# Performance work log

Hardware: AMD Instinct MI355X
Metric: run time of the kernel (lower is better)

Reference implementation:

```python
import jax, jax.numpy as jnp
import numpy as np

NEG_SLOPE = 0.2  # PyG GATConv default negative_slope


def gat_conv(x, src, dst, num_nodes, W, att_src, att_dst, bias, heads, out_ch, concat):
    """PyG-style GATConv (eval mode, self-loops already included in src/dst).
    x: [N, in]; W: [in, heads*out_ch]; att_*: [heads, out_ch]; bias: [heads*out_ch] or [out_ch].
    """
    N = num_nodes
    h = (x @ W).reshape(N, heads, out_ch)                      # [N, H, C]
    a_src = jnp.sum(h * att_src[None], axis=-1)                 # [N, H]
    a_dst = jnp.sum(h * att_dst[None], axis=-1)                 # [N, H]
    e = a_src[src] + a_dst[dst]                                 # [E, H]
    e = jnp.where(e > 0, e, NEG_SLOPE * e)                      # leaky_relu
    # segment softmax over incoming edges of each destination node
    m = jax.ops.segment_max(e, dst, num_segments=N)             # [N, H]
    w = jnp.exp(e - m[dst])                                     # [E, H]
    denom = jax.ops.segment_sum(w, dst, num_segments=N)         # [N, H]
    alpha = w / denom[dst]                                      # [E, H]
    out = jax.ops.segment_sum(h[src] * alpha[:, :, None], dst, num_segments=N)  # [N, H, C]
    if concat:
        out = out.reshape(N, heads * out_ch)
    else:
        out = out.mean(axis=1)
    return out + bias


def setup_inputs() -> dict:
    key = jax.random.key(0)
    ks = jax.random.split(key, 20)
    N, T, F_IN = 100000, 50, 10
    E = 1600000
    H1, C1 = 4, 32          # conv1: heads=4, hidden=32 -> 128
    LAT = 64                # latent_dim

    def g(k, shape, scale):
        return (jax.random.normal(k, shape, dtype=jnp.float32) * scale)

    inp = {
        "temporal_data": jax.random.normal(ks[0], (N, T, F_IN), dtype=jnp.float32),
        "x": jax.random.normal(ks[1], (N, F_IN), dtype=jnp.float32),
        "edge_index": jax.random.randint(ks[2], (2, E), 0, N, dtype=jnp.int32),
        # temporal encoder: Linear(10,64) -> ReLU -> Linear(64,64)
        "tW1": g(ks[3], (F_IN, 64), 0.3), "tb1": jnp.zeros((64,), jnp.float32),
        "tW2": g(ks[4], (64, LAT), 0.12), "tb2": jnp.zeros((LAT,), jnp.float32),
        # GATConv1: in=10, out=32, heads=4, concat
        "gW1": g(ks[5], (F_IN, H1 * C1), 0.3),
        "ga1_src": g(ks[6], (H1, C1), 0.17), "ga1_dst": g(ks[7], (H1, C1), 0.17),
        "gb1": jnp.zeros((H1 * C1,), jnp.float32),
        # GATConv2: in=128, out=64, heads=1, concat=False
        "gW2": g(ks[8], (H1 * C1, LAT), 0.09),
        "ga2_src": g(ks[9], (1, LAT), 0.12), "ga2_dst": g(ks[10], (1, LAT), 0.12),
        "gb2": jnp.zeros((LAT,), jnp.float32),
        # classifier: Linear(128,64) -> ReLU -> (Dropout eval) -> Linear(64,1) -> Sigmoid
        "cW1": g(ks[11], (2 * LAT, 64), 0.09), "cb1": jnp.zeros((64,), jnp.float32),
        "cW2": g(ks[12], (64, 1), 0.12), "cb2": jnp.zeros((1,), jnp.float32),
    }
    return inp


def reference(temporal_data, x, edge_index, tW1, tb1, tW2, tb2,
              gW1, ga1_src, ga1_dst, gb1, gW2, ga2_src, ga2_dst, gb2,
              cW1, cb1, cW2, cb2):
    N = x.shape[0]
    # temporal encoder then mean over time axis (dim=1)
    t = jax.nn.relu(temporal_data @ tW1 + tb1) @ tW2 + tb2      # [N, T, 64]
    t = t.mean(axis=1)                                           # [N, 64]
    # add self-loops (PyG GATConv default add_self_loops=True)
    loop = jnp.arange(N, dtype=edge_index.dtype)
    src = jnp.concatenate([edge_index[0], loop])
    dst = jnp.concatenate([edge_index[1], loop])
    h = gat_conv(x, src, dst, N, gW1, ga1_src, ga1_dst, gb1, heads=4, out_ch=32, concat=True)
    h = jax.nn.elu(h)
    g = gat_conv(h, src, dst, N, gW2, ga2_src, ga2_dst, gb2, heads=1, out_ch=64, concat=False)  # [N, 64]
    combined = jnp.concatenate([t, g], axis=-1)                  # [N, 128]
    z = jax.nn.relu(combined @ cW1 + cb1) @ cW2 + cb2            # [N, 1]
    return jax.nn.sigmoid(z)
```

## Files before the change

### kernel.cpp

```cpp
#include <hip/hip_runtime.h>
#include <hip/hip_bf16.h>

#define DEV_INLINE __device__ __forceinline__

typedef __attribute__((ext_vector_type(8))) short short8v;
typedef __attribute__((ext_vector_type(4))) float f32x4;

DEV_INLINE float lrelu(float v) { return fmaxf(v, 0.2f * v); }

DEV_INLINE unsigned int cvt_pk_bf16(float lo, float hi) {
    unsigned int r;
    asm("v_cvt_pk_bf16_f32 %0, %1, %2" : "=v"(r) : "v"(lo), "v"(hi));
    return r;
}

DEV_INLINE unsigned short f2bf_rne(float f) {
    unsigned int b = __float_as_uint(f);
    return (unsigned short)((b + 0x7FFFu + ((b >> 16) & 1u)) >> 16);
}

DEV_INLINE unsigned int pack_bf16(float lo, float hi) {
    return (unsigned int)f2bf_rne(lo) | ((unsigned int)f2bf_rne(hi) << 16);
}

DEV_INLINE float bf_lo(unsigned int u) { return __uint_as_float(u << 16); }
DEV_INLINE float bf_hi(unsigned int u) { return __uint_as_float(u & 0xFFFF0000u); }

__global__ __launch_bounds__(1024) void k_scan1(const int* __restrict__ counts,
                                                int* __restrict__ rowptr,
                                                int* __restrict__ partials, int N) {
    __shared__ int sd[1024];
    int li = threadIdx.x;
    int i  = blockIdx.x * 1024 + li;
    int v  = (i < N) ? counts[i] : 0;
    sd[li] = v;
    __syncthreads();
    for (int off = 1; off < 1024; off <<= 1) {
        int t = (li >= off) ? sd[li - off] : 0;
        __syncthreads();
        sd[li] += t;
        __syncthreads();
    }
    int inc = sd[li];
    if (i < N) rowptr[i + 1] = inc;
    if (li == 1023) partials[blockIdx.x] = inc;
}

__global__ void k_scan3(int* __restrict__ rowptr, const int* __restrict__ partials,
                        int* __restrict__ nxt, int N) {
    int i = blockIdx.x * blockDim.x + threadIdx.x;
    if (i > N) return;
    int v;
    if (i == 0) { v = 0; rowptr[0] = 0; }
    else {
        int blk = (i - 1) >> 10;
        int pp = 0;
        for (int b = 0; b < blk; ++b) pp += partials[b];
        v = rowptr[i] + pp;
        rowptr[i] = v;
    }
    if (i < N) nxt[i] = v;
}

#define SC_K 8
#define SC_P 16
__global__ __launch_bounds__(256) void k_scatter(const int* __restrict__ ei,
                                                 int* __restrict__ nxt,
                                                 int* __restrict__ col,
                                                 int E, int range) {
    int t = threadIdx.x;
    int base = blockIdx.x * (256 * SC_K);
    int s[SC_K], d[SC_K];
#pragma unroll
    for (int k = 0; k < SC_K; ++k) {
        int e = base + k * 256 + t;
        bool v = (e < E);
        s[k] = v ? ei[e] : 0;
        d[k] = v ? ei[E + e] : -1;
    }
    int lo = 0;
    for (int p = 0; p < SC_P; ++p, lo += range) {
        int hi = lo + range;
#pragma unroll
        for (int k = 0; k < SC_K; ++k) {
            if (d[k] >= lo && d[k] < hi) {
                int pos = atomicAdd(&nxt[d[k]], 1);
                col[pos] = s[k];
            }
        }
        __syncthreads();
    }
}

__global__ __launch_bounds__(256) void k_temporal(const float* __restrict__ td,
                                                  const float* __restrict__ tW1,
                                                  const float* __restrict__ tb1,
                                                  const int* __restrict__ ei,
                                                  int* __restrict__ counts,
                                                  const float* __restrict__ tW2,
                                                  const float* __restrict__ cW1,
                                                  const float* __restrict__ tb2,
                                                  const float* __restrict__ cb1,
                                                  unsigned short* __restrict__ Wf,
                                                  float* __restrict__ bcf,
                                                  unsigned short* __restrict__ mb,
                                                  int N, int E) {
    __shared__ float lds[4][512];
    int tid = threadIdx.x, lane = tid & 63, wv = tid >> 6;
    int gid = blockIdx.x * 256 + tid;

    int estr = gridDim.x * 256;
    for (int e = gid; e < E; e += estr) atomicAdd(&counts[ei[E + e]], 1);

    if (gid < 4096) {
        int i = gid >> 6, c = gid & 63;
        float s = 0.f;
#pragma unroll 8
        for (int k = 0; k < 64; ++k) s = fmaf(tW2[i * 64 + k], cW1[k * 64 + c], s);
        Wf[gid] = f2bf_rne(s);
    } else if (gid < 8192) {
        Wf[gid] = f2bf_rne(cW1[gid]);
    } else if (gid < 8256) {
        int c = gid - 8192;
        float s = cb1[c];
#pragma unroll 8
        for (int k = 0; k < 64; ++k) s = fmaf(tb2[k], cW1[k * 64 + c], s);
        bcf[c] = s;
    }

    int wid  = blockIdx.x * 4 + wv;
    int nwav = gridDim.x * 4;
    int col  = lane & 15;
    int g    = lane >> 4;

    int chunk = (N + nwav - 1) / nwav;
    int n0 = wid * chunk;
    int n1 = min(n0 + chunk, N);
    if (n0 >= n1) return;

    short8v B[4];
#pragma unroll
    for (int cb = 0; cb < 4; ++cb) {
        union { short8v v; unsigned short u[8]; } bu;
#pragma unroll
        for (int j = 0; j < 8; ++j) {
            int f = g * 8 + j;
            int c = cb * 16 + col;
            float w = (f < 10) ? tW1[f * 64 + c] : ((f == 10) ? tb1[c] : 0.f);
            bu.u[j] = f2bf_rne(w);
        }
        B[cb] = bu.v;
    }

    float* wb = lds[wv];

    const float4* r4 = reinterpret_cast<const float4*>(td + (size_t)n0 * 500);
    float4 va = r4[lane];
    float4 vb = (lane < 61) ? r4[64 + lane] : make_float4(0.f, 0.f, 0.f, 0.f);

    for (int n = n0; n < n1; ++n) {
        *reinterpret_cast<float4*>(wb + 4 * lane) = va;
        if (lane < 61) *reinterpret_cast<float4*>(wb + 256 + 4 * lane) = vb;

        if (n + 1 < n1) {
            const float4* rn = reinterpret_cast<const float4*>(td + (size_t)(n + 1) * 500);
            va = rn[lane];
            if (lane < 61) vb = rn[64 + lane];
        }

        float sum0 = 0.f, sum1 = 0.f, sum2 = 0.f, sum3 = 0.f;
#pragma unroll
        for (int tt = 0; tt < 4; ++tt) {
            int t = tt * 16 + col;
            bool valid = (t < 50);
            float x0 = 0.f, x1 = 0.f, x2 = 0.f, x3 = 0.f;
            float x4 = 0.f, x5 = 0.f, x6 = 0.f, x7 = 0.f;
            const float* rp = wb + t * 10;
            if (g == 0 && valid) {
                float2 p0 = *reinterpret_cast<const float2*>(rp);
                float2 p1 = *reinterpret_cast<const float2*>(rp + 2);
                float2 p2 = *reinterpret_cast<const float2*>(rp + 4);
                float2 p3 = *reinterpret_cast<const float2*>(rp + 6);
                x0 = p0.x; x1 = p0.y; x2 = p1.x; x3 = p1.y;
                x4 = p2.x; x5 = p2.y; x6 = p3.x; x7 = p3.y;
            } else if (g == 1 && valid) {
                float2 p4 = *reinterpret_cast<const float2*>(rp + 8);
                x0 = p4.x; x1 = p4.y; x2 = 1.0f;
            }
            union { short8v v; unsigned int w[4]; } au;
            au.w[0] = cvt_pk_bf16(x0, x1);
            au.w[1] = cvt_pk_bf16(x2, x3);
            au.w[2] = cvt_pk_bf16(x4, x5);
            au.w[3] = cvt_pk_bf16(x6, x7);

            f32x4 z = {0.f, 0.f, 0.f, 0.f};
            f32x4 c0 = __builtin_amdgcn_mfma_f32_16x16x32_bf16(au.v, B[0], z, 0, 0, 0);
            f32x4 c1 = __builtin_amdgcn_mfma_f32_16x16x32_bf16(au.v, B[1], z, 0, 0, 0);
            f32x4 c2 = __builtin_amdgcn_mfma_f32_16x16x32_bf16(au.v, B[2], z, 0, 0, 0);
            f32x4 c3 = __builtin_amdgcn_mfma_f32_16x16x32_bf16(au.v, B[3], z, 0, 0, 0);
#pragma unroll
            for (int i = 0; i < 4; ++i) {
                sum0 += fmaxf(c0[i], 0.f);
                sum1 += fmaxf(c1[i], 0.f);
                sum2 += fmaxf(c2[i], 0.f);
                sum3 += fmaxf(c3[i], 0.f);
            }
        }
        sum0 += __shfl_xor(sum0, 16); sum0 += __shfl_xor(sum0, 32);
        sum1 += __shfl_xor(sum1, 16); sum1 += __shfl_xor(sum1, 32);
        sum2 += __shfl_xor(sum2, 16); sum2 += __shfl_xor(sum2, 32);
        sum3 += __shfl_xor(sum3, 16); sum3 += __shfl_xor(sum3, 32);
        float mv = (g == 0) ? sum0 : (g == 1) ? sum1 : (g == 2) ? sum2 : sum3;
        mb[(size_t)n * 64 + lane] = f2bf_rne(mv * 0.02f);
    }
}

__global__ __launch_bounds__(256) void k_g1a(const float* __restrict__ x,
                                             const float* __restrict__ gW1,
                                             const float* __restrict__ as_w,
                                             const float* __restrict__ ad_w,
                                             unsigned short* __restrict__ h1b,
                                             float* __restrict__ a1s,
                                             float* __restrict__ a1d, int N) {
    int tid = threadIdx.x, lane = tid & 63;
    int n0 = blockIdx.x * 4 + (tid >> 6);
    int n  = __builtin_amdgcn_readfirstlane(n0 < N ? n0 : N - 1);

    float wa[10], wb[10];
#pragma unroll
    for (int i = 0; i < 10; ++i) { wa[i] = gW1[i * 128 + lane]; wb[i] = gW1[i * 128 + 64 + lane]; }
    const float* xp = x + (size_t)n * 10;
    float ha = 0.f, hb = 0.f;
#pragma unroll
    for (int i = 0; i < 10; ++i) { float xv = xp[i]; ha = fmaf(xv, wa[i], ha); hb = fmaf(xv, wb[i], hb); }

    int c = lane & 31;
    int headA = lane >> 5;
    float ps_a = ha * as_w[headA * 32 + c];
    float ps_b = hb * as_w[(headA + 2) * 32 + c];
    float pd_a = ha * ad_w[headA * 32 + c];
    float pd_b = hb * ad_w[(headA + 2) * 32 + c];
#pragma unroll
    for (int m = 1; m < 32; m <<= 1) {
        ps_a += __shfl_xor(ps_a, m); ps_b += __shfl_xor(ps_b, m);
        pd_a += __shfl_xor(pd_a, m); pd_b += __shfl_xor(pd_b, m);
    }
    if (n0 < N) {
        h1b[(size_t)n * 128 + lane]      = f2bf_rne(ha);
        h1b[(size_t)n * 128 + 64 + lane] = f2bf_rne(hb);
        if (c == 0) {
            a1s[n * 4 + headA]     = ps_a;
            a1s[n * 4 + 2 + headA] = ps_b;
            a1d[n * 4 + headA]     = pd_a;
            a1d[n * 4 + 2 + headA] = pd_b;
        }
    }
}

__global__ __launch_bounds__(256) void k_g1b(const int* __restrict__ rowptr,
                                             const int* __restrict__ col,
                                             const unsigned int* __restrict__ h1u,
                                             const float* __restrict__ a1s,
                                             const float* __restrict__ a1d,
                                             const float* __restrict__ gb1,
                                             unsigned int* __restrict__ out1u, int N) {
    int tid = threadIdx.x, lane = tid & 63;
    int n0 = blockIdx.x * 4 + (tid >> 6);
    int n  = __builtin_amdgcn_readfirstlane(n0 < N ? n0 : N - 1);

    int start = rowptr[n], end = rowptr[n + 1];
    int h = lane >> 5;
    int c = lane & 31;
    int hsel = c >> 3;
    float advh = a1d[n * 4 + hsel];
    const uint2* h1u2 = reinterpret_cast<const uint2*>(h1u);

    float den = 0.f, a0 = 0.f, a1v = 0.f, a2v = 0.f, a3v = 0.f;
    if (h == 0) {
        float w = __expf(lrelu(a1s[n * 4 + hsel] + advh));
        uint2 u = h1u2[(size_t)n * 32 + c];
        den = w;
        a0 = w * bf_lo(u.x); a1v = w * bf_hi(u.x);
        a2v = w * bf_lo(u.y); a3v = w * bf_hi(u.y);
    }
    int e = start + h;
    for (; e + 2 < end; e += 4) {
        int s0 = col[e], s1 = col[e + 2];
        float q0 = a1s[s0 * 4 + hsel];
        float q1 = a1s[s1 * 4 + hsel];
        uint2 u0 = h1u2[(size_t)s0 * 32 + c];
        uint2 u1 = h1u2[(size_t)s1 * 32 + c];
        float w0 = __expf(lrelu(q0 + advh));
        float w1 = __expf(lrelu(q1 + advh));
        den += w0 + w1;
        a0 = fmaf(w0, bf_lo(u0.x), a0); a1v = fmaf(w0, bf_hi(u0.x), a1v);
        a2v = fmaf(w0, bf_lo(u0.y), a2v); a3v = fmaf(w0, bf_hi(u0.y), a3v);
        a0 = fmaf(w1, bf_lo(u1.x), a0); a1v = fmaf(w1, bf_hi(u1.x), a1v);
        a2v = fmaf(w1, bf_lo(u1.y), a2v); a3v = fmaf(w1, bf_hi(u1.y), a3v);
    }
    if (e < end) {
        int s = col[e];
        float q = a1s[s * 4 + hsel];
        uint2 u = h1u2[(size_t)s * 32 + c];
        float w = __expf(lrelu(q + advh));
        den += w;
        a0 = fmaf(w, bf_lo(u.x), a0); a1v = fmaf(w, bf_hi(u.x), a1v);
        a2v = fmaf(w, bf_lo(u.y), a2v); a3v = fmaf(w, bf_hi(u.y), a3v);
    }
    den += __shfl_xor(den, 32);
    a0  += __shfl_xor(a0, 32);  a1v += __shfl_xor(a1v, 32);
    a2v += __shfl_xor(a2v, 32); a3v += __shfl_xor(a3v, 32);

    if (n0 < N && h == 0) {
        float inv = 1.f / den;
        float v0 = a0 * inv + gb1[4 * c + 0];
        float v1 = a1v * inv + gb1[4 * c + 1];
        float v2 = a2v * inv + gb1[4 * c + 2];
        float v3 = a3v * inv + gb1[4 * c + 3];
        v0 = (v0 > 0.f) ? v0 : (__expf(v0) - 1.f);
        v1 = (v1 > 0.f) ? v1 : (__expf(v1) - 1.f);
        v2 = (v2 > 0.f) ? v2 : (__expf(v2) - 1.f);
        v3 = (v3 > 0.f) ? v3 : (__expf(v3) - 1.f);
        uint2 o; o.x = pack_bf16(v0, v1); o.y = pack_bf16(v2, v3);
        *reinterpret_cast<uint2*>(out1u + (size_t)n * 64 + 2 * c) = o;
    }
}

__global__ __launch_bounds__(256) void k_g2a(const unsigned short* __restrict__ out1b,
                                             const float* __restrict__ gW2,
                                             const float* __restrict__ a2sw,
                                             const float* __restrict__ a2dw,
                                             unsigned short* __restrict__ h2b,
                                             float* __restrict__ a2s,
                                             float* __restrict__ a2d, int N) {
    int lane = threadIdx.x & 63;
    int wid  = (blockIdx.x * blockDim.x + threadIdx.x) >> 6;
    int nwav = (gridDim.x * blockDim.x) >> 6;
    int col = lane & 15, g4 = lane >> 4;

    short8v Bf[4][4];
#pragma unroll
    for (int ks = 0; ks < 4; ++ks)
#pragma unroll
        for (int cb = 0; cb < 4; ++cb) {
            union { short8v v; unsigned short u[8]; } bu;
#pragma unroll
            for (int j = 0; j < 8; ++j)
                bu.u[j] = f2bf_rne(gW2[(ks * 32 + g4 * 8 + j) * 64 + cb * 16 + col]);
            Bf[ks][cb] = bu.v;
        }
    float asv[4], adv[4];
#pragma unroll
    for (int cb = 0; cb < 4; ++cb) { asv[cb] = a2sw[cb * 16 + col]; adv[cb] = a2dw[cb * 16 + col]; }

    int ntile = (N + 15) >> 4;
    for (int t = wid; t < ntile; t += nwav) {
        int n0 = t * 16;
        int node = n0 + col; if (node >= N) node = N - 1;
        const unsigned short* xr = out1b + (size_t)node * 128;
        f32x4 acc0 = {0.f, 0.f, 0.f, 0.f}, acc1 = acc0, acc2 = acc0, acc3 = acc0;
#pragma unroll
        for (int ks = 0; ks < 4; ++ks) {
            short8v a = *reinterpret_cast<const short8v*>(xr + ks * 32 + g4 * 8);
            acc0 = __builtin_amdgcn_mfma_f32_16x16x32_bf16(a, Bf[ks][0], acc0, 0, 0, 0);
            acc1 = __builtin_amdgcn_mfma_f32_16x16x32_bf16(a, Bf[ks][1], acc1, 0, 0, 0);
            acc2 = __builtin_amdgcn_mfma_f32_16x16x32_bf16(a, Bf[ks][2], acc2, 0, 0, 0);
            acc3 = __builtin_amdgcn_mfma_f32_16x16x32_bf16(a, Bf[ks][3], acc3, 0, 0, 0);
        }
        float ps[4] = {0.f, 0.f, 0.f, 0.f}, pd[4] = {0.f, 0.f, 0.f, 0.f};
#define G2A_EPI(CB, ACC)                                                      \
        {                                                                     \
            _Pragma("unroll")                                                 \
            for (int i = 0; i < 4; ++i) {                                     \
                float v = ACC[i];                                             \
                int r = n0 + g4 * 4 + i;                                      \
                if (r < N) h2b[(size_t)r * 64 + CB * 16 + col] = f2bf_rne(v); \
                ps[i] = fmaf(v, asv[CB], ps[i]);                              \
                pd[i] = fmaf(v, adv[CB], pd[i]);                              \
            }                                                                 \
        }
        G2A_EPI(0, acc0) G2A_EPI(1, acc1) G2A_EPI(2, acc2) G2A_EPI(3, acc3)
#undef G2A_EPI
#pragma unroll
        for (int i = 0; i < 4; ++i) {
            ps[i] += __shfl_xor(ps[i], 1); ps[i] += __shfl_xor(ps[i], 2);
            ps[i] += __shfl_xor(ps[i], 4); ps[i] += __shfl_xor(ps[i], 8);
            pd[i] += __shfl_xor(pd[i], 1); pd[i] += __shfl_xor(pd[i], 2);
            pd[i] += __shfl_xor(pd[i], 4); pd[i] += __shfl_xor(pd[i], 8);
        }
        if (col == 0) {
#pragma unroll
            for (int i = 0; i < 4; ++i) {
                int r = n0 + g4 * 4 + i;
                if (r < N) { a2s[r] = ps[i]; a2d[r] = pd[i]; }
            }
        }
    }
}

__global__ __launch_bounds__(256) void k_g2b(const int* __restrict__ rowptr,
                                             const int* __restrict__ col,
                                             const unsigned int* __restrict__ h2u,
                                             const float* __restrict__ a2s,
                                             const float* __restrict__ a2d,
                                             const float* __restrict__ gb2,
                                             unsigned int* __restrict__ gu, int N) {
    int tid = threadIdx.x, lane = tid & 63;
    int n0 = blockIdx.x * 4 + (tid >> 6);
    int n  = __builtin_amdgcn_readfirstlane(n0 < N ? n0 : N - 1);

    int start = rowptr[n], end = rowptr[n + 1];
    int q = lane >> 4, c = lane & 15;
    float ad = a2d[n];
    const uint2* h2u2 = reinterpret_cast<const uint2*>(h2u);

    float den = 0.f, a0 = 0.f, a1v = 0.f, a2v = 0.f, a3v = 0.f;
    if (q == 0) {
        float w = __expf(lrelu(a2s[n] + ad));
        uint2 u = h2u2[(size_t)n * 16 + c];
        den = w;
        a0 = w * bf_lo(u.x); a1v = w * bf_hi(u.x);
        a2v = w * bf_lo(u.y); a3v = w * bf_hi(u.y);
    }
    int e = start + q;
    for (; e + 4 < end; e += 8) {
        int s0 = col[e], s1 = col[e + 4];
        float q0 = a2s[s0], q1 = a2s[s1];
        uint2 u0 = h2u2[(size_t)s0 * 16 + c];
        uint2 u1 = h2u2[(size_t)s1 * 16 + c];
        float w0 = __expf(lrelu(q0 + ad));
        float w1 = __expf(lrelu(q1 + ad));
        den += w0 + w1;
        a0 = fmaf(w0, bf_lo(u0.x), a0); a1v = fmaf(w0, bf_hi(u0.x), a1v);
        a2v = fmaf(w0, bf_lo(u0.y), a2v); a3v = fmaf(w0, bf_hi(u0.y), a3v);
        a0 = fmaf(w1, bf_lo(u1.x), a0); a1v = fmaf(w1, bf_hi(u1.x), a1v);
        a2v = fmaf(w1, bf_lo(u1.y), a2v); a3v = fmaf(w1, bf_hi(u1.y), a3v);
    }
    if (e < end) {
        int s = col[e];
        float w = __expf(lrelu(a2s[s] + ad));
        uint2 u = h2u2[(size_t)s * 16 + c];
        den += w;
        a0 = fmaf(w, bf_lo(u.x), a0); a1v = fmaf(w, bf_hi(u.x), a1v);
        a2v = fmaf(w, bf_lo(u.y), a2v); a3v = fmaf(w, bf_hi(u.y), a3v);
    }
    den += __shfl_xor(den, 16); den += __shfl_xor(den, 32);
    a0  += __shfl_xor(a0, 16);  a0  += __shfl_xor(a0, 32);
    a1v += __shfl_xor(a1v, 16); a1v += __shfl_xor(a1v, 32);
    a2v += __shfl_xor(a2v, 16); a2v += __shfl_xor(a2v, 32);
    a3v += __shfl_xor(a3v, 16); a3v += __shfl_xor(a3v, 32);

    if (n0 < N && lane < 16) {
        float inv = 1.f / den;
        uint2 o;
        o.x = pack_bf16(a0 * inv + gb2[4 * c + 0], a1v * inv + gb2[4 * c + 1]);
        o.y = pack_bf16(a2v * inv + gb2[4 * c + 2], a3v * inv + gb2[4 * c + 3]);
        *reinterpret_cast<uint2*>(gu + (size_t)n * 32 + 2 * c) = o;
    }
}

__global__ __launch_bounds__(256) void k_cls(const unsigned short* __restrict__ mb,
                                             const unsigned short* __restrict__ gb,
                                             const unsigned short* __restrict__ Wf,
                                             const float* __restrict__ bc,
                                             const float* __restrict__ cW2,
                                             const float* __restrict__ cb2,
                                             float* __restrict__ out, int N) {
    int lane = threadIdx.x & 63;
    int wid  = (blockIdx.x * blockDim.x + threadIdx.x) >> 6;
    int nwav = (gridDim.x * blockDim.x) >> 6;
    int col = lane & 15, g4 = lane >> 4;

    short8v Bf[4][4];
#pragma unroll
    for (int ks = 0; ks < 4; ++ks)
#pragma unroll
        for (int cb = 0; cb < 4; ++cb) {
            union { short8v v; unsigned short u[8]; } bu;
#pragma unroll
            for (int j = 0; j < 8; ++j)
                bu.u[j] = Wf[(ks * 32 + g4 * 8 + j) * 64 + cb * 16 + col];
            Bf[ks][cb] = bu.v;
        }
    float w2v[4], bcv[4];
#pragma unroll
    for (int cb = 0; cb < 4; ++cb) { w2v[cb] = cW2[cb * 16 + col]; bcv[cb] = bc[cb * 16 + col]; }
    float cb2v = cb2[0];

    int ntile = (N + 15) >> 4;
    for (int t = wid; t < ntile; t += nwav) {
        int n0 = t * 16;
        int node = n0 + col; if (node >= N) node = N - 1;
        const unsigned short* mr = mb + (size_t)node * 64;
        const unsigned short* gr = gb + (size_t)node * 64;
        f32x4 acc0 = {0.f, 0.f, 0.f, 0.f}, acc1 = acc0, acc2 = acc0, acc3 = acc0;
#pragma unroll
        for (int ks = 0; ks < 4; ++ks) {
            short8v a = (ks < 2)
                ? *reinterpret_cast<const short8v*>(mr + ks * 32 + g4 * 8)
                : *reinterpret_cast<const short8v*>(gr + (ks - 2) * 32 + g4 * 8);
            acc0 = __builtin_amdgcn_mfma_f32_16x16x32_bf16(a, Bf[ks][0], acc0, 0, 0, 0);
            acc1 = __builtin_amdgcn_mfma_f32_16x16x32_bf16(a, Bf[ks][1], acc1, 0, 0, 0);
            acc2 = __builtin_amdgcn_mfma_f32_16x16x32_bf16(a, Bf[ks][2], acc2, 0, 0, 0);
            acc3 = __builtin_amdgcn_mfma_f32_16x16x32_bf16(a, Bf[ks][3], acc3, 0, 0, 0);
        }
        float z[4] = {0.f, 0.f, 0.f, 0.f};
#define CLS_EPI(CB, ACC)                                                   \
        {                                                                  \
            _Pragma("unroll")                                              \
            for (int i = 0; i < 4; ++i)                                    \
                z[i] = fmaf(fmaxf(ACC[i] + bcv[CB], 0.f), w2v[CB], z[i]);  \
        }
        CLS_EPI(0, acc0) CLS_EPI(1, acc1) CLS_EPI(2, acc2) CLS_EPI(3, acc3)
#undef CLS_EPI
#pragma unroll
        for (int i = 0; i < 4; ++i) {
            z[i] += __shfl_xor(z[i], 1); z[i] += __shfl_xor(z[i], 2);
            z[i] += __shfl_xor(z[i], 4); z[i] += __shfl_xor(z[i], 8);
        }
        if (col == 0) {
#pragma unroll
            for (int i = 0; i < 4; ++i) {
                int r = n0 + g4 * 4 + i;
                if (r < N) out[r] = 1.f / (1.f + __expf(-(z[i] + cb2v)));
            }
        }
    }
}

extern "C" void kernel_launch(void* const* d_in, const int* in_sizes, int n_in,
                              void* d_out, int out_size, void* d_ws, size_t ws_size,
                              hipStream_t stream) {
    const float* td   = (const float*)d_in[0];
    const float* x    = (const float*)d_in[1];
    const int*   ei   = (const int*)d_in[2];
    const float* tW1  = (const float*)d_in[3];
    const float* tb1  = (const float*)d_in[4];
    const float* tW2  = (const float*)d_in[5];
    const float* tb2  = (const float*)d_in[6];
    const float* gW1  = (const float*)d_in[7];
    const float* ga1s = (const float*)d_in[8];
    const float* ga1d = (const float*)d_in[9];
    const float* gb1  = (const float*)d_in[10];
    const float* gW2  = (const float*)d_in[11];
    const float* ga2s = (const float*)d_in[12];
    const float* ga2d = (const float*)d_in[13];
    const float* gb2  = (const float*)d_in[14];
    const float* cW1  = (const float*)d_in[15];
    const float* cb1  = (const float*)d_in[16];
    const float* cW2  = (const float*)d_in[17];
    const float* cb2  = (const float*)d_in[18];

    int N = in_sizes[1] / 10;
    int E = in_sizes[2] / 2;

    float* fws = (float*)d_ws;
    unsigned short* mb16   = (unsigned short*)fws;
    unsigned short* h1b    = (unsigned short*)(fws + (size_t)N * 32);
    unsigned short* out1b  = (unsigned short*)(fws + (size_t)N * 96);
    float* a1s   = fws + (size_t)N * 160;
    float* a1d   = fws + (size_t)N * 164;
    unsigned short* h2b = h1b;
    float* a2s   = a1s;
    float* a2d   = a1d;
    unsigned short* gb16 = out1b;

    int* ib       = (int*)(fws + (size_t)N * 168);
    int* counts   = ib;
    int* rowptr   = ib + N;
    int* nxt      = ib + 2 * N + 1;
    int* partials = ib + 3 * N + 1;
    int* col      = ib + 3 * N + 1 + 128;

    unsigned short* Wf = (unsigned short*)(col + E);
    float* bcf = (float*)(Wf + 8192);

    hipMemsetAsync(counts, 0, (size_t)N * sizeof(int), stream);

    int NB = (N + 1023) / 1024;
    int range = (N + SC_P - 1) / SC_P;
    int nb4   = (N + 3) / 4;
    int ntile = (N + 15) / 16;
    int nbt   = (ntile + 3) / 4;

    k_temporal<<<2048, 256, 0, stream>>>(td, tW1, tb1, ei, counts,
                                         tW2, cW1, tb2, cb1, Wf, bcf, mb16, N, E);
    k_scan1  <<<NB, 1024, 0, stream>>>(counts, rowptr, partials, N);
    k_scan3  <<<(N + 1 + 255) / 256, 256, 0, stream>>>(rowptr, partials, nxt, N);
    k_scatter<<<(E + 256 * SC_K - 1) / (256 * SC_K), 256, 0, stream>>>(ei, nxt, col, E, range);

    k_g1a<<<nb4, 256, 0, stream>>>(x, gW1, ga1s, ga1d, h1b, a1s, a1d, N);
    k_g1b<<<nb4, 256, 0, stream>>>(rowptr, col, (const unsigned int*)h1b, a1s, a1d, gb1,
                                   (unsigned int*)out1b, N);
    k_g2a<<<nbt, 256, 0, stream>>>(out1b, gW2, ga2s, ga2d, h2b, a2s, a2d, N);
    k_g2b<<<nb4, 256, 0, stream>>>(rowptr, col, (const unsigned int*)h2b, a2s, a2d, gb2,
                                   (unsigned int*)gb16, N);
    k_cls<<<nbt, 256, 0, stream>>>(mb16, gb16, Wf, bcf, cW2, cb2, (float*)d_out, N);
}
```

Measured before the change: 404.6 us.

## Double-buffer temporal LDS staging and widen GAT gather loads to 16 bytes

The temporal encoder now stages rows in two LDS buffers per wave and prefetches two rows ahead, so the write for row n+1 and the global load for row n+2 overlap compute on row n. Both GAT aggregation kernels switch from 8-byte to 16-byte per-lane gathers, so each lane holds 8 channels and more edges are processed in parallel per wave (4 edge slots in layer 1, 8 in layer 2). This adds accumulator registers and extra shuffle-reduction steps. The layer-2 loop also drops its 2-way unroll.

```diff
diff --git a/kernel.cpp b/kernel.cpp
--- a/kernel.cpp
+++ b/kernel.cpp
@@ -105,7 +105,7 @@
                                                   float* __restrict__ bcf,
                                                   unsigned short* __restrict__ mb,
                                                   int N, int E) {
-    __shared__ float lds[4][512];
+    __shared__ float lds[4][2][512];
     int tid = threadIdx.x, lane = tid & 63, wv = tid >> 6;
     int gid = blockIdx.x * 256 + tid;
 
@@ -137,6 +137,7 @@
     int n0 = wid * chunk;
     int n1 = min(n0 + chunk, N);
     if (n0 >= n1) return;
+    int cnt = n1 - n0;
 
     short8v B[4];
 #pragma unroll
@@ -152,18 +153,34 @@
         B[cb] = bu.v;
     }
 
-    float* wb = lds[wv];
-
-    const float4* r4 = reinterpret_cast<const float4*>(td + (size_t)n0 * 500);
-    float4 va = r4[lane];
-    float4 vb = (lane < 61) ? r4[64 + lane] : make_float4(0.f, 0.f, 0.f, 0.f);
-
-    for (int n = n0; n < n1; ++n) {
-        *reinterpret_cast<float4*>(wb + 4 * lane) = va;
-        if (lane < 61) *reinterpret_cast<float4*>(wb + 256 + 4 * lane) = vb;
-
-        if (n + 1 < n1) {
-            const float4* rn = reinterpret_cast<const float4*>(td + (size_t)(n + 1) * 500);
+    float* buf0 = lds[wv][0];
+    float* buf1 = lds[wv][1];
+
+    {
+        const float4* r4 = reinterpret_cast<const float4*>(td + (size_t)n0 * 500);
+        float4 va = r4[lane];
+        float4 vb = (lane < 61) ? r4[64 + lane] : make_float4(0.f, 0.f, 0.f, 0.f);
+        *reinterpret_cast<float4*>(buf0 + 4 * lane) = va;
+        if (lane < 61) *reinterpret_cast<float4*>(buf0 + 256 + 4 * lane) = vb;
+    }
+    float4 va = make_float4(0.f, 0.f, 0.f, 0.f), vb = va;
+    if (cnt > 1) {
+        const float4* rn = reinterpret_cast<const float4*>(td + (size_t)(n0 + 1) * 500);
+        va = rn[lane];
+        if (lane < 61) vb = rn[64 + lane];
+    }
+
+    for (int i = 0; i < cnt; ++i) {
+        int n = n0 + i;
+        float* wb  = (i & 1) ? buf1 : buf0;
+        float* wbn = (i & 1) ? buf0 : buf1;
+
+        if (i + 1 < cnt) {
+            *reinterpret_cast<float4*>(wbn + 4 * lane) = va;
+            if (lane < 61) *reinterpret_cast<float4*>(wbn + 256 + 4 * lane) = vb;
+        }
+        if (i + 2 < cnt) {
+            const float4* rn = reinterpret_cast<const float4*>(td + (size_t)(n + 2) * 500);
             va = rn[lane];
             if (lane < 61) vb = rn[64 + lane];
         }
@@ -199,11 +216,11 @@
             f32x4 c2 = __builtin_amdgcn_mfma_f32_16x16x32_bf16(au.v, B[2], z, 0, 0, 0);
             f32x4 c3 = __builtin_amdgcn_mfma_f32_16x16x32_bf16(au.v, B[3], z, 0, 0, 0);
 #pragma unroll
-            for (int i = 0; i < 4; ++i) {
-                sum0 += fmaxf(c0[i], 0.f);
-                sum1 += fmaxf(c1[i], 0.f);
-                sum2 += fmaxf(c2[i], 0.f);
-                sum3 += fmaxf(c3[i], 0.f);
+            for (int i2 = 0; i2 < 4; ++i2) {
+                sum0 += fmaxf(c0[i2], 0.f);
+                sum1 += fmaxf(c1[i2], 0.f);
+                sum2 += fmaxf(c2[i2], 0.f);
+                sum3 += fmaxf(c3[i2], 0.f);
             }
         }
         sum0 += __shfl_xor(sum0, 16); sum0 += __shfl_xor(sum0, 32);
@@ -269,60 +286,80 @@
     int n  = __builtin_amdgcn_readfirstlane(n0 < N ? n0 : N - 1);
 
     int start = rowptr[n], end = rowptr[n + 1];
-    int h = lane >> 5;
-    int c = lane & 31;
-    int hsel = c >> 3;
+    int q = lane >> 4, c = lane & 15;
+    int hsel = c >> 2;
     float advh = a1d[n * 4 + hsel];
-    const uint2* h1u2 = reinterpret_cast<const uint2*>(h1u);
-
-    float den = 0.f, a0 = 0.f, a1v = 0.f, a2v = 0.f, a3v = 0.f;
-    if (h == 0) {
+    const uint4* h1q = reinterpret_cast<const uint4*>(h1u);
+
+    float den = 0.f;
+    float a0 = 0.f, a1v = 0.f, a2v = 0.f, a3v = 0.f;
+    float a4 = 0.f, a5 = 0.f, a6 = 0.f, a7 = 0.f;
+    if (q == 0) {
         float w = __expf(lrelu(a1s[n * 4 + hsel] + advh));
-        uint2 u = h1u2[(size_t)n * 32 + c];
+        uint4 u = h1q[(size_t)n * 16 + c];
         den = w;
         a0 = w * bf_lo(u.x); a1v = w * bf_hi(u.x);
         a2v = w * bf_lo(u.y); a3v = w * bf_hi(u.y);
-    }
-    int e = start + h;
-    for (; e + 2 < end; e += 4) {
-        int s0 = col[e], s1 = col[e + 2];
+        a4 = w * bf_lo(u.z); a5 = w * bf_hi(u.z);
+        a6 = w * bf_lo(u.w); a7 = w * bf_hi(u.w);
+    }
+    int e = start + q;
+    for (; e + 4 < end; e += 8) {
+        int s0 = col[e], s1 = col[e + 4];
         float q0 = a1s[s0 * 4 + hsel];
         float q1 = a1s[s1 * 4 + hsel];
-        uint2 u0 = h1u2[(size_t)s0 * 32 + c];
-        uint2 u1 = h1u2[(size_t)s1 * 32 + c];
+        uint4 u0 = h1q[(size_t)s0 * 16 + c];
+        uint4 u1 = h1q[(size_t)s1 * 16 + c];
         float w0 = __expf(lrelu(q0 + advh));
         float w1 = __expf(lrelu(q1 + advh));
         den += w0 + w1;
         a0 = fmaf(w0, bf_lo(u0.x), a0); a1v = fmaf(w0, bf_hi(u0.x), a1v);
         a2v = fmaf(w0, bf_lo(u0.y), a2v); a3v = fmaf(w0, bf_hi(u0.y), a3v);
+        a4 = fmaf(w0, bf_lo(u0.z), a4); a5 = fmaf(w0, bf_hi(u0.z), a5);
+        a6 = fmaf(w0, bf_lo(u0.w), a6); a7 = fmaf(w0, bf_hi(u0.w), a7);
         a0 = fmaf(w1, bf_lo(u1.x), a0); a1v = fmaf(w1, bf_hi(u1.x), a1v);
         a2v = fmaf(w1, bf_lo(u1.y), a2v); a3v = fmaf(w1, bf_hi(u1.y), a3v);
+        a4 = fmaf(w1, bf_lo(u1.z), a4); a5 = fmaf(w1, bf_hi(u1.z), a5);
+        a6 = fmaf(w1, bf_lo(u1.w), a6); a7 = fmaf(w1, bf_hi(u1.w), a7);
     }
     if (e < end) {
         int s = col[e];
-        float q = a1s[s * 4 + hsel];
-        uint2 u = h1u2[(size_t)s * 32 + c];
-        float w = __expf(lrelu(q + advh));
+        float qv = a1s[s * 4 + hsel];
+        uint4 u = h1q[(size_t)s * 16 + c];
+        float w = __expf(lrelu(qv + advh));
         den += w;
         a0 = fmaf(w, bf_lo(u.x), a0); a1v = fmaf(w, bf_hi(u.x), a1v);
         a2v = fmaf(w, bf_lo(u.y), a2v); a3v = fmaf(w, bf_hi(u.y), a3v);
-    }
-    den += __shfl_xor(den, 32);
-    a0  += __shfl_xor(a0, 32);  a1v += __shfl_xor(a1v, 32);
-    a2v += __shfl_xor(a2v, 32); a3v += __shfl_xor(a3v, 32);
-
-    if (n0 < N && h == 0) {
+        a4 = fmaf(w, bf_lo(u.z), a4); a5 = fmaf(w, bf_hi(u.z), a5);
+        a6 = fmaf(w, bf_lo(u.w), a6); a7 = fmaf(w, bf_hi(u.w), a7);
+    }
+#define RED2(v) v += __shfl_xor(v, 16); v += __shfl_xor(v, 32);
+    RED2(den) RED2(a0) RED2(a1v) RED2(a2v) RED2(a3v)
+    RED2(a4) RED2(a5) RED2(a6) RED2(a7)
+#undef RED2
+
+    if (n0 < N && lane < 16) {
         float inv = 1.f / den;
-        float v0 = a0 * inv + gb1[4 * c + 0];
-        float v1 = a1v * inv + gb1[4 * c + 1];
-        float v2 = a2v * inv + gb1[4 * c + 2];
-        float v3 = a3v * inv + gb1[4 * c + 3];
+        float v0 = a0 * inv + gb1[8 * c + 0];
+        float v1 = a1v * inv + gb1[8 * c + 1];
+        float v2 = a2v * inv + gb1[8 * c + 2];
+        float v3 = a3v * inv + gb1[8 * c + 3];
+        float v4 = a4 * inv + gb1[8 * c + 4];
+        float v5 = a5 * inv + gb1[8 * c + 5];
+        float v6 = a6 * inv + gb1[8 * c + 6];
+        float v7 = a7 * inv + gb1[8 * c + 7];
         v0 = (v0 > 0.f) ? v0 : (__expf(v0) - 1.f);
         v1 = (v1 > 0.f) ? v1 : (__expf(v1) - 1.f);
         v2 = (v2 > 0.f) ? v2 : (__expf(v2) - 1.f);
         v3 = (v3 > 0.f) ? v3 : (__expf(v3) - 1.f);
-        uint2 o; o.x = pack_bf16(v0, v1); o.y = pack_bf16(v2, v3);
-        *reinterpret_cast<uint2*>(out1u + (size_t)n * 64 + 2 * c) = o;
+        v4 = (v4 > 0.f) ? v4 : (__expf(v4) - 1.f);
+        v5 = (v5 > 0.f) ? v5 : (__expf(v5) - 1.f);
+        v6 = (v6 > 0.f) ? v6 : (__expf(v6) - 1.f);
+        v7 = (v7 > 0.f) ? v7 : (__expf(v7) - 1.f);
+        uint4 o;
+        o.x = pack_bf16(v0, v1); o.y = pack_bf16(v2, v3);
+        o.z = pack_bf16(v4, v5); o.w = pack_bf16(v6, v7);
+        *reinterpret_cast<uint4*>(out1u + (size_t)n * 64 + 4 * c) = o;
     }
 }
 
@@ -410,52 +447,45 @@
     int n  = __builtin_amdgcn_readfirstlane(n0 < N ? n0 : N - 1);
 
     int start = rowptr[n], end = rowptr[n + 1];
-    int q = lane >> 4, c = lane & 15;
+    int q = lane >> 3, c = lane & 7;
     float ad = a2d[n];
-    const uint2* h2u2 = reinterpret_cast<const uint2*>(h2u);
-
-    float den = 0.f, a0 = 0.f, a1v = 0.f, a2v = 0.f, a3v = 0.f;
+    const uint4* h2q = reinterpret_cast<const uint4*>(h2u);
+
+    float den = 0.f;
+    float a0 = 0.f, a1v = 0.f, a2v = 0.f, a3v = 0.f;
+    float a4 = 0.f, a5 = 0.f, a6 = 0.f, a7 = 0.f;
     if (q == 0) {
         float w = __expf(lrelu(a2s[n] + ad));
-        uint2 u = h2u2[(size_t)n * 16 + c];
+        uint4 u = h2q[(size_t)n * 8 + c];
         den = w;
         a0 = w * bf_lo(u.x); a1v = w * bf_hi(u.x);
         a2v = w * bf_lo(u.y); a3v = w * bf_hi(u.y);
-    }
-    int e = start + q;
-    for (; e + 4 < end; e += 8) {
-        int s0 = col[e], s1 = col[e + 4];
-        float q0 = a2s[s0], q1 = a2s[s1];
-        uint2 u0 = h2u2[(size_t)s0 * 16 + c];
-        uint2 u1 = h2u2[(size_t)s1 * 16 + c];
-        float w0 = __expf(lrelu(q0 + ad));
-        float w1 = __expf(lrelu(q1 + ad));
-        den += w0 + w1;
-        a0 = fmaf(w0, bf_lo(u0.x), a0); a1v = fmaf(w0, bf_hi(u0.x), a1v);
-        a2v = fmaf(w0, bf_lo(u0.y), a2v); a3v = fmaf(w0, bf_hi(u0.y), a3v);
-        a0 = fmaf(w1, bf_lo(u1.x), a0); a1v = fmaf(w1, bf_hi(u1.x), a1v);
-        a2v = fmaf(w1, bf_lo(u1.y), a2v); a3v = fmaf(w1, bf_hi(u1.y), a3v);
-    }
-    if (e < end) {
+        a4 = w * bf_lo(u.z); a5 = w * bf_hi(u.z);
+        a6 = w * bf_lo(u.w); a7 = w * bf_hi(u.w);
+    }
+    for (int e = start + q; e < end; e += 8) {
         int s = col[e];
         float w = __expf(lrelu(a2s[s] + ad));
-        uint2 u = h2u2[(size_t)s * 16 + c];
+        uint4 u = h2q[(size_t)s * 8 + c];
         den += w;
         a0 = fmaf(w, bf_lo(u.x), a0); a1v = fmaf(w, bf_hi(u.x), a1v);
         a2v = fmaf(w, bf_lo(u.y), a2v); a3v = fmaf(w, bf_hi(u.y), a3v);
-    }
-    den += __shfl_xor(den, 16); den += __shfl_xor(den, 32);
-    a0  += __shfl_xor(a0, 16);  a0  += __shfl_xor(a0, 32);
-    a1v += __shfl_xor(a1v, 16); a1v += __shfl_xor(a1v, 32);
-    a2v += __shfl_xor(a2v, 16); a2v += __shfl_xor(a2v, 32);
-    a3v += __shfl_xor(a3v, 16); a3v += __shfl_xor(a3v, 32);
-
-    if (n0 < N && lane < 16) {
+        a4 = fmaf(w, bf_lo(u.z), a4); a5 = fmaf(w, bf_hi(u.z), a5);
+        a6 = fmaf(w, bf_lo(u.w), a6); a7 = fmaf(w, bf_hi(u.w), a7);
+    }
+#define RED3(v) v += __shfl_xor(v, 8); v += __shfl_xor(v, 16); v += __shfl_xor(v, 32);
+    RED3(den) RED3(a0) RED3(a1v) RED3(a2v) RED3(a3v)
+    RED3(a4) RED3(a5) RED3(a6) RED3(a7)
+#undef RED3
+
+    if (n0 < N && lane < 8) {
         float inv = 1.f / den;
-        uint2 o;
-        o.x = pack_bf16(a0 * inv + gb2[4 * c + 0], a1v * inv + gb2[4 * c + 1]);
-        o.y = pack_bf16(a2v * inv + gb2[4 * c + 2], a3v * inv + gb2[4 * c + 3]);
-        *reinterpret_cast<uint2*>(gu + (size_t)n * 32 + 2 * c) = o;
+        uint4 o;
+        o.x = pack_bf16(a0 * inv + gb2[8 * c + 0], a1v * inv + gb2[8 * c + 1]);
+        o.y = pack_bf16(a2v * inv + gb2[8 * c + 2], a3v * inv + gb2[8 * c + 3]);
+        o.z = pack_bf16(a4 * inv + gb2[8 * c + 4], a5 * inv + gb2[8 * c + 5]);
+        o.w = pack_bf16(a6 * inv + gb2[8 * c + 6], a7 * inv + gb2[8 * c + 7]);
+        *reinterpret_cast<uint4*>(gu + (size_t)n * 32 + 4 * c) = o;
     }
 }
 
```

Result: no change. 399.2 us (-1.3%).
